# Kernel optimization log

Measured on AMD Instinct MI355X. Metric: run time of the kernel, lower is better.

## Reference

```python
import jax, jax.numpy as jnp
import numpy as np

NEG_INF_SCALE = -1e9


def setup_inputs() -> dict:
    key = jax.random.key(0)
    ks = jax.random.split(key, 8)
    B, T, M, D = 64, 1024, 256, 1024
    query = jax.random.normal(ks[0], (B, 1, M), dtype=jnp.float32)
    keys = jax.random.normal(ks[1], (B, T, M), dtype=jnp.float32)
    values = jax.random.normal(ks[2], (B, T, D), dtype=jnp.float32)
    mask = jax.random.randint(ks[3], (B, 1, T), 0, 2).astype(jnp.float32)
    # MLP params (scaled like torch default init ~ 1/sqrt(fan_in))
    W1 = jax.random.normal(ks[4], (4 * M, D), dtype=jnp.float32) / np.sqrt(4 * M)
    b1 = jnp.zeros((D,), dtype=jnp.float32)
    W2 = jax.random.normal(ks[5], (D, D), dtype=jnp.float32) / np.sqrt(D)
    b2 = jnp.zeros((D,), dtype=jnp.float32)
    w_score = jax.random.normal(ks[6], (D, 1), dtype=jnp.float32) / np.sqrt(D)
    b_score = jnp.zeros((1,), dtype=jnp.float32)
    return {"query": query, "keys": keys, "values": values, "mask": mask,
            "W1": W1, "b1": b1, "W2": W2, "b2": b2,
            "w_score": w_score, "b_score": b_score}


def reference(query, keys, values, mask, W1, b1, W2, b2, w_score, b_score):
    # query: [B,1,M] broadcast against keys: [B,T,M]
    q = jnp.broadcast_to(query, keys.shape)
    att_input = jnp.concatenate([q, keys, q - keys, q * keys], axis=-1)  # [B,T,4M]
    h = jax.nn.relu(att_input @ W1 + b1)   # [B,T,D]
    h = jax.nn.relu(h @ W2 + b2)           # [B,T,D]
    score = h @ w_score + b_score          # [B,T,1]
    logits = jnp.swapaxes(score, 1, 2)     # [B,1,T]
    logits = logits + mask * NEG_INF_SCALE
    attn = jax.nn.softmax(logits, axis=-1)  # [B,1,T]
    out = jnp.matmul(attn, values)          # [B,1,D]
    return out
```

## Files before the change

kernel.cpp:

```cpp
#include <hip/hip_runtime.h>

#define DEV __device__ __forceinline__

typedef __attribute__((ext_vector_type(4))) float f32x4;
typedef __attribute__((ext_vector_type(8))) short short8;
typedef __attribute__((ext_vector_type(4))) short s16x4;
typedef __attribute__((ext_vector_type(4))) float f32x4v;

DEV short f2bf(float f) {
  union { float f; unsigned u; } v; v.f = f;
  unsigned r = (v.u + 0x7FFFu + ((v.u >> 16) & 1u)) >> 16;
  return (short)r;
}

DEV void gload16(const void* g, void* l) {
  __builtin_amdgcn_global_load_lds(
      (const __attribute__((address_space(1))) void*)g,
      (__attribute__((address_space(3))) void*)l, 16, 0, 0);
}

#define BAR() __builtin_amdgcn_s_barrier()
#define LGKMW(n)                                              \
  {                                                           \
    asm volatile("s_waitcnt lgkmcnt(" #n ")" ::: "memory");   \
    __builtin_amdgcn_sched_barrier(0);                        \
  }
#define VMW(n)                                                \
  {                                                           \
    asm volatile("s_waitcnt vmcnt(" #n ")" ::: "memory");     \
    __builtin_amdgcn_sched_barrier(0);                        \
  }


__global__ __launch_bounds__(256) void k_prep_keys(const float* __restrict__ k,
                                                   short* __restrict__ o) {
  int i = (blockIdx.x * 256 + threadIdx.x) * 8;
  f32x4v v0 = *(const f32x4v*)(k + i);
  f32x4v v1 = *(const f32x4v*)(k + i + 4);
  short8 s;
  s[0] = f2bf(v0[0]); s[1] = f2bf(v0[1]); s[2] = f2bf(v0[2]); s[3] = f2bf(v0[3]);
  s[4] = f2bf(v1[0]); s[5] = f2bf(v1[1]); s[6] = f2bf(v1[2]); s[7] = f2bf(v1[3]);
  *(short8*)(o + i) = s;
}

__global__ __launch_bounds__(256) void k_prep_w2f(const float* __restrict__ w2,
                                                  short* __restrict__ w2f) {
  __shared__ float tile[64][65];
  const int kt = blockIdx.x, n0 = blockIdx.y * 64;
  const int a = threadIdx.x & 63, q = threadIdx.x >> 6;
#pragma unroll
  for (int i = 0; i < 16; ++i) {
    int kk = i * 4 + q;
    tile[kk][a] = w2[(size_t)(kt * 64 + kk) * 1024 + n0 + a];
  }
  __syncthreads();
  const int l = threadIdx.x & 63, cgl = threadIdx.x >> 6;
#pragma unroll
  for (int kh = 0; kh < 2; ++kh) {
    short8 v;
#pragma unroll
    for (int j = 0; j < 8; ++j)
      v[j] = f2bf(tile[kh * 32 + (l >> 4) * 8 + j][cgl * 16 + (l & 15)]);
    *(short8*)&w2f[((size_t)((kt * 2 + kh) * 64 + (n0 >> 4) + cgl)) * 512 + l * 8] = v;
  }
}

__global__ __launch_bounds__(256) void k_prep_wkt(const float* __restrict__ w1,
                                                  const float* __restrict__ query,
                                                  const float* __restrict__ b1,
                                                  short* __restrict__ wktf,
                                                  float* __restrict__ biasb) {
  __shared__ short tile[64][264];
  __shared__ float redm[64][4];
  const int b = blockIdx.x, d0 = blockIdx.y * 64;
  const int d = threadIdx.x & 63, mq = threadIdx.x >> 6;
  float bacc = 0.f;
#pragma unroll 4
  for (int i = 0; i < 64; ++i) {
    int m = i * 4 + mq;
    float qv = query[b * 256 + m];
    float wa = w1[(size_t)m * 1024 + d0 + d];
    float wb = w1[(size_t)(256 + m) * 1024 + d0 + d];
    float wc = w1[(size_t)(512 + m) * 1024 + d0 + d];
    float wd = w1[(size_t)(768 + m) * 1024 + d0 + d];
    tile[d][m] = f2bf(wb - wc + qv * wd);
    bacc += qv * (wa + wc);
  }
  redm[d][mq] = bacc;
  __syncthreads();
  const int l = threadIdx.x & 63, cgl = threadIdx.x >> 6;
  short* ob = wktf + (size_t)b * 262144;
#pragma unroll
  for (int kt = 0; kt < 4; ++kt)
#pragma unroll
    for (int kh = 0; kh < 2; ++kh) {
      short8 v = *(const short8*)&tile[cgl * 16 + (l & 15)]
                                      [kt * 64 + kh * 32 + (l >> 4) * 8];
      *(short8*)&ob[((size_t)((kt * 2 + kh) * 64 + (d0 >> 4) + cgl)) * 512 + l * 8] = v;
    }
  if (threadIdx.x < 64) {
    int dd = threadIdx.x;
    biasb[b * 1024 + d0 + dd] =
        redm[dd][0] + redm[dd][1] + redm[dd][2] + redm[dd][3] + b1[d0 + dd];
  }
}


template <int MODE>
__global__ __launch_bounds__(256, 2) void k_gemm(const short* __restrict__ A,
                                                 const short* __restrict__ Bf,
                                                 const float* __restrict__ bias,
                                                 const float* __restrict__ wscore,
                                                 short* __restrict__ hout,
                                                 float* __restrict__ spart) {
  __shared__ short lds[32768];
  constexpr int SK = (MODE == 1) ? 256 : 1024;
  constexpr int KT = (MODE == 1) ? 4 : 16;

  const int tid = threadIdx.x;
  const int bx = blockIdx.x;
  const int L = (bx & 7) * 256 + (bx >> 3);

  const short *Ab, *Bb;
  const float *biasp, *wsp = nullptr;
  short* houtp = nullptr;
  int rt, ct;
  if constexpr (MODE == 1) {
    const int b = L >> 5;
    rt = (L >> 2) & 7; ct = L & 3;
    Ab = A + ((size_t)(b * 1024 + rt * 128)) * 256;
    Bb = Bf + (size_t)b * 262144;
    biasp = bias + b * 1024 + ct * 256;
    houtp = hout + ((size_t)(b * 1024 + rt * 128)) * 1024 + ct * 256;
  } else {
    rt = L >> 2; ct = L & 3;
    Ab = A + (size_t)rt * 128 * 1024;
    Bb = Bf;
    biasp = bias + ct * 256;
    wsp = wscore + ct * 256;
  }

  int gA[4], dA[4];
#pragma unroll
  for (int j = 0; j < 4; ++j) {
    int s = tid + j * 256, row = s >> 3, kc = (s & 7) ^ (row & 7);
    gA[j] = row * SK + kc * 8;
    dA[j] = s * 8;
  }
  auto STAGE = [&](int kt) {
    const int bb = (kt & 3) * 8192;
#pragma unroll
    for (int j = 0; j < 4; ++j) gload16(Ab + gA[j] + kt * 64, &lds[bb + dA[j]]);
  };

  const int lane = tid & 63, l15 = lane & 15, l4 = lane >> 4, wc = tid >> 6;
  const int afo0 = l15 * 64 + ((l4 ^ (l15 & 7)) * 8);
  const int afo1 = l15 * 64 + (((4 + l4) ^ (l15 & 7)) * 8);

  f32x4 acc[8][4];
#pragma unroll
  for (int m = 0; m < 8; ++m)
#pragma unroll
    for (int n = 0; n < 4; ++n) acc[m][n] = f32x4{0.f, 0.f, 0.f, 0.f};
  short8 bf[2][4][2];
  short8 af[8];

#define LOADB(kt, BK_)                                                          \
  _Pragma("unroll") for (int n_ = 0; n_ < 4; ++n_) {                            \
    _Pragma("unroll") for (int kh_ = 0; kh_ < 2; ++kh_) {                       \
      bf[BK_][n_][kh_] = *(const short8*)(Bb +                                  \
          ((size_t)(((kt) * 2 + kh_) * 64 + ct * 16 + n_ * 4 + wc) << 9) +      \
          lane * 8);                                                            \
    }                                                                           \
  }

  STAGE(0);
  LOADB(0, 0);
  STAGE(1);
  STAGE(2);
  VMW(8);
  BAR();

#pragma unroll
  for (int t = 0; t < KT; ++t) {
    const int bb = (t & 3) * 8192;
    if (t + 1 < KT) LOADB(t + 1, (t + 1) & 1);
#pragma unroll
    for (int m = 0; m < 8; ++m) af[m] = *(const short8*)&lds[bb + afo0 + m * 1024];
    LGKMW(0);
    __builtin_amdgcn_s_setprio(1);
#pragma unroll
    for (int m = 0; m < 8; ++m)
#pragma unroll
      for (int n = 0; n < 4; ++n)
        acc[m][n] = __builtin_amdgcn_mfma_f32_16x16x32_bf16(bf[t & 1][n][0], af[m],
                                                            acc[m][n], 0, 0, 0);
    __builtin_amdgcn_s_setprio(0);
#pragma unroll
    for (int m = 0; m < 8; ++m) af[m] = *(const short8*)&lds[bb + afo1 + m * 1024];
    if (t + 3 < KT) STAGE(t + 3);
    LGKMW(0);
    __builtin_amdgcn_s_setprio(1);
#pragma unroll
    for (int m = 0; m < 8; ++m)
#pragma unroll
      for (int n = 0; n < 4; ++n)
        acc[m][n] = __builtin_amdgcn_mfma_f32_16x16x32_bf16(bf[t & 1][n][1], af[m],
                                                            acc[m][n], 0, 0, 0);
    __builtin_amdgcn_s_setprio(0);
    if (t + 3 < KT) {
      VMW(4);
    } else {
      VMW(0);
    }
    BAR();
  }
#undef LOADB

  if constexpr (MODE == 1) {
    float bv[4][4];
#pragma unroll
    for (int n = 0; n < 4; ++n)
#pragma unroll
      for (int r2 = 0; r2 < 4; ++r2)
        bv[n][r2] = biasp[n * 64 + wc * 16 + l4 * 4 + r2];
#pragma unroll
    for (int m = 0; m < 8; ++m) {
      int row = m * 16 + l15;
#pragma unroll
      for (int n = 0; n < 4; ++n) {
        s16x4 pk;
#pragma unroll
        for (int r2 = 0; r2 < 4; ++r2)
          pk[r2] = f2bf(fmaxf(acc[m][n][r2] + bv[n][r2], 0.f));
        *(s16x4*)&houtp[(size_t)row * 1024 + n * 64 + wc * 16 + l4 * 4] = pk;
      }
    }
  } else {
    float bv[4][4], wv[4][4];
#pragma unroll
    for (int n = 0; n < 4; ++n)
#pragma unroll
      for (int r2 = 0; r2 < 4; ++r2) {
        int c = n * 64 + wc * 16 + l4 * 4 + r2;
        bv[n][r2] = biasp[c];
        wv[n][r2] = wsp[c];
      }
    float* so = spart + ((size_t)(ct * 4 + wc) << 16) + rt * 128;
#pragma unroll
    for (int m = 0; m < 8; ++m) {
      float s = 0.f;
#pragma unroll
      for (int n = 0; n < 4; ++n)
#pragma unroll
        for (int r2 = 0; r2 < 4; ++r2)
          s += fmaxf(acc[m][n][r2] + bv[n][r2], 0.f) * wv[n][r2];
      s += __shfl_xor(s, 16);
      s += __shfl_xor(s, 32);
      if (lane < 16) so[m * 16 + l15] = s;
    }
  }
}


__global__ __launch_bounds__(256) void k_softmax(const float* __restrict__ spart,
                                                 const float* __restrict__ mask,
                                                 const float* __restrict__ bscore,
                                                 float* __restrict__ attn) {
  const int b = blockIdx.x, tid = threadIdx.x;
  __shared__ float sm[1024];
  __shared__ float red[8];
  const float bs = bscore[0];
  float lmax = -3.0e38f;
  for (int t = tid; t < 1024; t += 256) {
    float s = bs;
#pragma unroll
    for (int c = 0; c < 16; ++c) s += spart[(size_t)c * 65536 + b * 1024 + t];
    float lg = s + mask[b * 1024 + t] * (-1e9f);
    sm[t] = lg;
    lmax = fmaxf(lmax, lg);
  }
  for (int o = 32; o; o >>= 1) lmax = fmaxf(lmax, __shfl_xor(lmax, o));
  const int wid = tid >> 6, lane = tid & 63;
  if (lane == 0) red[wid] = lmax;
  __syncthreads();
  float bmax = fmaxf(fmaxf(red[0], red[1]), fmaxf(red[2], red[3]));
  float lsum = 0.f;
  for (int t = tid; t < 1024; t += 256) {
    float e = __expf(sm[t] - bmax);
    sm[t] = e;
    lsum += e;
  }
  for (int o = 32; o; o >>= 1) lsum += __shfl_xor(lsum, o);
  __syncthreads();
  if (lane == 0) red[wid] = lsum;
  __syncthreads();
  float inv = 1.0f / (red[0] + red[1] + red[2] + red[3]);
  for (int t = tid; t < 1024; t += 256) attn[b * 1024 + t] = sm[t] * inv;
}

__global__ __launch_bounds__(256) void k_out(const float* __restrict__ attn,
                                             const float* __restrict__ values,
                                             float* __restrict__ part) {
  const int b = blockIdx.x >> 3, ts = blockIdx.x & 7;
  const int tid = threadIdx.x;
  __shared__ float at[128];
  if (tid < 128) at[tid] = attn[b * 1024 + ts * 128 + tid];
  __syncthreads();
  const float* vb = values + ((size_t)b * 1024 + ts * 128) * 1024 + tid * 4;
  f32x4 acc = {0.f, 0.f, 0.f, 0.f};
#pragma unroll 8
  for (int t = 0; t < 128; ++t) {
    f32x4v v = *(const f32x4v*)(vb + (size_t)t * 1024);
    float a = at[t];
    acc[0] += a * v[0]; acc[1] += a * v[1]; acc[2] += a * v[2]; acc[3] += a * v[3];
  }
  *(f32x4*)(part + ((size_t)(b * 8 + ts)) * 1024 + tid * 4) = acc;
}

__global__ __launch_bounds__(256) void k_red(const float* __restrict__ part,
                                             float* __restrict__ out) {
  const int b = blockIdx.x;
  const int c4 = threadIdx.x * 4;
  f32x4 s = {0.f, 0.f, 0.f, 0.f};
#pragma unroll
  for (int ts = 0; ts < 8; ++ts) {
    f32x4v v = *(const f32x4v*)(part + ((size_t)(b * 8 + ts)) * 1024 + c4);
    s[0] += v[0]; s[1] += v[1]; s[2] += v[2]; s[3] += v[3];
  }
  *(f32x4*)(out + b * 1024 + c4) = s;
}


extern "C" void kernel_launch(void* const* d_in, const int* in_sizes, int n_in,
                              void* d_out, int out_size, void* d_ws, size_t ws_size,
                              hipStream_t stream) {
  const float* query  = (const float*)d_in[0];
  const float* keys   = (const float*)d_in[1];
  const float* values = (const float*)d_in[2];
  const float* mask   = (const float*)d_in[3];
  const float* W1     = (const float*)d_in[4];
  const float* b1     = (const float*)d_in[5];
  const float* W2     = (const float*)d_in[6];
  const float* b2     = (const float*)d_in[7];
  const float* wscore = (const float*)d_in[8];
  const float* bscore = (const float*)d_in[9];
  float* out = (float*)d_out;

  char* ws = (char*)d_ws;
  short* keysb = (short*)(ws);
  short* wktf  = (short*)(ws + 33554432ull);
  short* w2f   = (short*)(ws + 67108864ull);
  float* biasb = (float*)(ws + 69206016ull);
  short* h1    = (short*)(ws + 69468160ull);
  float* spart = (float*)(ws + 203685888ull);
  float* attn  = (float*)(ws + 207880192ull);
  float* part  = (float*)(ws + 208142336ull);

  k_prep_keys<<<8192, 256, 0, stream>>>(keys, keysb);
  k_prep_w2f<<<dim3(16, 16), 256, 0, stream>>>(W2, w2f);
  k_prep_wkt<<<dim3(64, 16), 256, 0, stream>>>(W1, query, b1, wktf, biasb);

  k_gemm<1><<<2048, 256, 0, stream>>>(keysb, wktf, biasb, nullptr, h1, nullptr);
  k_gemm<2><<<2048, 256, 0, stream>>>(h1, w2f, b2, wscore, nullptr, spart);

  k_softmax<<<64, 256, 0, stream>>>(spart, mask, bscore, attn);
  k_out<<<512, 256, 0, stream>>>(attn, values, part);
  k_red<<<64, 256, 0, stream>>>(part, out);
}
```

Baseline: 274.7 us.

## Shrink GEMM tiles to 128x128 with 2x2 wave grid and 3-stage LDS ring

Both MLP GEMMs switch from 128x256 output tiles with four column-split waves to 128x128 tiles with a 2x2 wave arrangement, doubling the grid to 4096 blocks. The LDS ring drops from four stages to three, and launch bounds ask for three blocks per CU, aiming for higher occupancy and better latency hiding. In exchange, the A operand is re-read from global memory twice as often. B fragments are now loaded within the same iteration instead of being prefetched one step ahead, which may expose global load latency before the MFMAs. The spart partial-score layout is remapped to match the new column and wave split.

```diff
diff --git a/kernel.cpp b/kernel.cpp
--- a/kernel.cpp
+++ b/kernel.cpp
@@ -107,37 +107,37 @@
 
 
 template <int MODE>
-__global__ __launch_bounds__(256, 2) void k_gemm(const short* __restrict__ A,
+__global__ __launch_bounds__(256, 3) void k_gemm(const short* __restrict__ A,
                                                  const short* __restrict__ Bf,
                                                  const float* __restrict__ bias,
                                                  const float* __restrict__ wscore,
                                                  short* __restrict__ hout,
                                                  float* __restrict__ spart) {
-  __shared__ short lds[32768];
+  __shared__ short lds[24576];
   constexpr int SK = (MODE == 1) ? 256 : 1024;
   constexpr int KT = (MODE == 1) ? 4 : 16;
 
   const int tid = threadIdx.x;
   const int bx = blockIdx.x;
-  const int L = (bx & 7) * 256 + (bx >> 3);
+  const int L = (bx & 7) * 512 + (bx >> 3);
 
   const short *Ab, *Bb;
   const float *biasp, *wsp = nullptr;
   short* houtp = nullptr;
   int rt, ct;
   if constexpr (MODE == 1) {
-    const int b = L >> 5;
-    rt = (L >> 2) & 7; ct = L & 3;
+    const int b = L >> 6;
+    rt = (L >> 3) & 7; ct = L & 7;
     Ab = A + ((size_t)(b * 1024 + rt * 128)) * 256;
     Bb = Bf + (size_t)b * 262144;
-    biasp = bias + b * 1024 + ct * 256;
-    houtp = hout + ((size_t)(b * 1024 + rt * 128)) * 1024 + ct * 256;
+    biasp = bias + b * 1024 + ct * 128;
+    houtp = hout + ((size_t)(b * 1024 + rt * 128)) * 1024 + ct * 128;
   } else {
-    rt = L >> 2; ct = L & 3;
+    rt = L >> 3; ct = L & 7;
     Ab = A + (size_t)rt * 128 * 1024;
     Bb = Bf;
-    biasp = bias + ct * 256;
-    wsp = wscore + ct * 256;
+    biasp = bias + ct * 128;
+    wsp = wscore + ct * 128;
   }
 
   int gA[4], dA[4];
@@ -148,67 +148,65 @@
     dA[j] = s * 8;
   }
   auto STAGE = [&](int kt) {
-    const int bb = (kt & 3) * 8192;
+    const int bb = (kt % 3) * 8192;
 #pragma unroll
     for (int j = 0; j < 4; ++j) gload16(Ab + gA[j] + kt * 64, &lds[bb + dA[j]]);
   };
 
-  const int lane = tid & 63, l15 = lane & 15, l4 = lane >> 4, wc = tid >> 6;
-  const int afo0 = l15 * 64 + ((l4 ^ (l15 & 7)) * 8);
-  const int afo1 = l15 * 64 + (((4 + l4) ^ (l15 & 7)) * 8);
-
-  f32x4 acc[8][4];
-#pragma unroll
-  for (int m = 0; m < 8; ++m)
+  const int lane = tid & 63, l15 = lane & 15, l4 = lane >> 4;
+  const int wid = tid >> 6, wr = wid >> 1, wc = wid & 1;
+  const int afo0 = (wr * 64 + l15) * 64 + ((l4 ^ (l15 & 7)) * 8);
+  const int afo1 = (wr * 64 + l15) * 64 + (((4 + l4) ^ (l15 & 7)) * 8);
+
+  f32x4 acc[4][4];
+#pragma unroll
+  for (int m = 0; m < 4; ++m)
 #pragma unroll
     for (int n = 0; n < 4; ++n) acc[m][n] = f32x4{0.f, 0.f, 0.f, 0.f};
-  short8 bf[2][4][2];
-  short8 af[8];
-
-#define LOADB(kt, BK_)                                                          \
+  short8 bf[4];
+  short8 af[4];
+
+#define LOADB(kt, kh_)                                                          \
   _Pragma("unroll") for (int n_ = 0; n_ < 4; ++n_) {                            \
-    _Pragma("unroll") for (int kh_ = 0; kh_ < 2; ++kh_) {                       \
-      bf[BK_][n_][kh_] = *(const short8*)(Bb +                                  \
-          ((size_t)(((kt) * 2 + kh_) * 64 + ct * 16 + n_ * 4 + wc) << 9) +      \
-          lane * 8);                                                            \
-    }                                                                           \
+    bf[n_] = *(const short8*)(Bb +                                              \
+        ((size_t)(((kt) * 2 + (kh_)) * 64 + ct * 8 + wc * 4 + n_) << 9) +       \
+        lane * 8);                                                              \
   }
 
   STAGE(0);
-  LOADB(0, 0);
   STAGE(1);
-  STAGE(2);
-  VMW(8);
+  VMW(4);
   BAR();
 
 #pragma unroll
   for (int t = 0; t < KT; ++t) {
-    const int bb = (t & 3) * 8192;
-    if (t + 1 < KT) LOADB(t + 1, (t + 1) & 1);
-#pragma unroll
-    for (int m = 0; m < 8; ++m) af[m] = *(const short8*)&lds[bb + afo0 + m * 1024];
+    const int bb = (t % 3) * 8192;
+    LOADB(t, 0);
+#pragma unroll
+    for (int m = 0; m < 4; ++m) af[m] = *(const short8*)&lds[bb + afo0 + m * 1024];
     LGKMW(0);
     __builtin_amdgcn_s_setprio(1);
 #pragma unroll
-    for (int m = 0; m < 8; ++m)
+    for (int m = 0; m < 4; ++m)
 #pragma unroll
       for (int n = 0; n < 4; ++n)
-        acc[m][n] = __builtin_amdgcn_mfma_f32_16x16x32_bf16(bf[t & 1][n][0], af[m],
+        acc[m][n] = __builtin_amdgcn_mfma_f32_16x16x32_bf16(bf[n], af[m],
                                                             acc[m][n], 0, 0, 0);
     __builtin_amdgcn_s_setprio(0);
-#pragma unroll
-    for (int m = 0; m < 8; ++m) af[m] = *(const short8*)&lds[bb + afo1 + m * 1024];
-    if (t + 3 < KT) STAGE(t + 3);
+    LOADB(t, 1);
+    if (t + 2 < KT) STAGE(t + 2);
+#pragma unroll
+    for (int m = 0; m < 4; ++m) af[m] = *(const short8*)&lds[bb + afo1 + m * 1024];
     LGKMW(0);
     __builtin_amdgcn_s_setprio(1);
 #pragma unroll
-    for (int m = 0; m < 8; ++m)
+    for (int m = 0; m < 4; ++m)
 #pragma unroll
       for (int n = 0; n < 4; ++n)
-        acc[m][n] = __builtin_amdgcn_mfma_f32_16x16x32_bf16(bf[t & 1][n][1], af[m],
+        acc[m][n] = __builtin_amdgcn_mfma_f32_16x16x32_bf16(bf[n], af[m],
                                                             acc[m][n], 0, 0, 0);
     __builtin_amdgcn_s_setprio(0);
-    if (t + 3 < KT) {
+    if (t + 2 < KT) {
       VMW(4);
     } else {
       VMW(0);
@@ -223,17 +221,17 @@
     for (int n = 0; n < 4; ++n)
 #pragma unroll
       for (int r2 = 0; r2 < 4; ++r2)
-        bv[n][r2] = biasp[n * 64 + wc * 16 + l4 * 4 + r2];
-#pragma unroll
-    for (int m = 0; m < 8; ++m) {
-      int row = m * 16 + l15;
+        bv[n][r2] = biasp[wc * 64 + n * 16 + l4 * 4 + r2];
+#pragma unroll
+    for (int m = 0; m < 4; ++m) {
+      int row = wr * 64 + m * 16 + l15;
 #pragma unroll
       for (int n = 0; n < 4; ++n) {
         s16x4 pk;
 #pragma unroll
         for (int r2 = 0; r2 < 4; ++r2)
           pk[r2] = f2bf(fmaxf(acc[m][n][r2] + bv[n][r2], 0.f));
-        *(s16x4*)&houtp[(size_t)row * 1024 + n * 64 + wc * 16 + l4 * 4] = pk;
+        *(s16x4*)&houtp[(size_t)row * 1024 + wc * 64 + n * 16 + l4 * 4] = pk;
       }
     }
   } else {
@@ -242,13 +240,13 @@
     for (int n = 0; n < 4; ++n)
 #pragma unroll
       for (int r2 = 0; r2 < 4; ++r2) {
-        int c = n * 64 + wc * 16 + l4 * 4 + r2;
+        int c = wc * 64 + n * 16 + l4 * 4 + r2;
         bv[n][r2] = biasp[c];
         wv[n][r2] = wsp[c];
       }
-    float* so = spart + ((size_t)(ct * 4 + wc) << 16) + rt * 128;
-#pragma unroll
-    for (int m = 0; m < 8; ++m) {
+    float* so = spart + ((size_t)(ct * 2 + wc) << 16) + rt * 128 + wr * 64;
+#pragma unroll
+    for (int m = 0; m < 4; ++m) {
       float s = 0.f;
 #pragma unroll
       for (int n = 0; n < 4; ++n)
@@ -361,8 +359,8 @@
   k_prep_w2f<<<dim3(16, 16), 256, 0, stream>>>(W2, w2f);
   k_prep_wkt<<<dim3(64, 16), 256, 0, stream>>>(W1, query, b1, wktf, biasb);
 
-  k_gemm<1><<<2048, 256, 0, stream>>>(keysb, wktf, biasb, nullptr, h1, nullptr);
-  k_gemm<2><<<2048, 256, 0, stream>>>(h1, w2f, b2, wscore, nullptr, spart);
+  k_gemm<1><<<4096, 256, 0, stream>>>(keysb, wktf, biasb, nullptr, h1, nullptr);
+  k_gemm<2><<<4096, 256, 0, stream>>>(h1, w2f, b2, wscore, nullptr, spart);
 
   k_softmax<<<64, 256, 0, stream>>>(spart, mask, bscore, attn);
   k_out<<<512, 256, 0, stream>>>(attn, values, part);
```

Result: slower. 295.3 us (+7.5%).
